# Optimization experiments

Measured on AMD Instinct MI355X. Metric: run time of the kernel, lower is better.

The kernel has to match this reference:

```python
import jax, jax.numpy as jnp
import numpy as np

B, N, M, D = 1, 16384, 16384, 3
CHUNK = 2048          # x tile size for the online-min KNN pass
NN_WEIGHT = 1.0       # self.nn_weight
# both_ways=False, free_weight=0, ch_normals_K=0 -> only cham_x branch is active


def setup_inputs() -> dict:
    key = jax.random.key(0)
    k1, k2, k3 = jax.random.split(key, 3)
    # LiDAR-like point clouds, scaled to a ~20 m scene extent
    pc1 = jax.random.normal(k1, (B, N, D), dtype=jnp.float32) * 10.0
    est_flow = jax.random.normal(k2, (B, N, D), dtype=jnp.float32) * 0.1
    pc2 = jax.random.normal(k3, (B, M, D), dtype=jnp.float32) * 10.0
    return {"pc1": pc1, "est_flow": est_flow, "pc2": pc2}


def _knn1_l1_dists(x, y):
    """Per-point min L1 distance from x [N,3] to y [M,3], tiled over x.

    Equivalent to knn_points(x, y, K=1, norm=1).dists[..., 0] without
    materializing the full [N, M] distance matrix.
    """
    n = x.shape[0]
    x_tiles = x.reshape(n // CHUNK, CHUNK, D)

    def tile_min(xc):  # xc: [CHUNK, 3]
        d = jnp.sum(jnp.abs(xc[:, None, :] - y[None, :, :]), axis=-1)  # [CHUNK, M]
        return jnp.min(d, axis=-1)                                     # [CHUNK]

    return jax.lax.map(tile_min, x_tiles).reshape(n)


def reference(pc1, est_flow, pc2):
    x = pc1 + est_flow                                   # deformed cloud [B,N,3]
    cham_x = jax.vmap(_knn1_l1_dists)(x, pc2)            # [B, N]
    cham_y = jnp.float32(0.0)                            # both_ways=False
    freespace_loss = jnp.zeros_like(cham_x)              # free_weight == 0 branch
    chamf_loss = NN_WEIGHT * (cham_x.mean() + cham_y)    # free_weight * 0 omitted
    return (chamf_loss, freespace_loss)
```

## Files before the change

### kernel.cpp

```cpp
#include <hip/hip_runtime.h>


#define TPB 256
#define RB 8
#define PTS_PER_BLOCK (TPB * RB)
#define YSEG 64
#define NITER (YSEG / 16)

typedef float sf16 __attribute__((ext_vector_type(16)));
typedef float sf8  __attribute__((ext_vector_type(8)));

#define SLOAD24(B16, B8, PTR, O16, O8)                                     \
  asm volatile("s_load_dwordx16 %0, %2, " O16 "\n\t"                       \
               "s_load_dwordx8  %1, %2, " O8                               \
               : "=s"(B16), "=s"(B8) : "s"(PTR));

#define SWAIT(B16, B8)                                                     \
  asm volatile("s_waitcnt lgkmcnt(0)" : "+s"(B16), "+s"(B8));

#define DIST2S(MR, AXv, AYv, AZv, Y0X, Y0Y, Y0Z, Y1X, Y1Y, Y1Z)           \
  {                                                                        \
    float t0, t1, t2, t3, t4;                                              \
    asm("v_sub_f32 %1, %9, %6\n\t"                                         \
        "v_sub_f32 %2, %10, %7\n\t"                                        \
        "v_sub_f32 %3, %11, %8\n\t"                                        \
        "v_sub_f32 %4, %12, %6\n\t"                                        \
        "v_sub_f32 %5, %13, %7\n\t"                                        \
        "v_add_f32 %1, |%1|, |%2|\n\t"                                     \
        "v_sub_f32 %2, %14, %8\n\t"                                        \
        "v_add_f32 %4, |%4|, |%5|\n\t"                                     \
        "v_add_f32 %1, %1, |%3|\n\t"                                       \
        "v_add_f32 %4, %4, |%2|\n\t"                                       \
        "v_min3_f32 %0, %0, %1, %4"                                        \
        : "+v"(MR), "=&v"(t0), "=&v"(t1), "=&v"(t2), "=&v"(t3), "=&v"(t4)  \
        : "v"(AXv), "v"(AYv), "v"(AZv),                                    \
          "s"(Y0X), "s"(Y0Y), "s"(Y0Z), "s"(Y1X), "s"(Y1Y), "s"(Y1Z));    \
  }

#define COMPUTE8(G16, G8)                                                  \
  {                                                                        \
    _Pragma("unroll")                                                      \
    for (int r = 0; r < RB; ++r)                                           \
      DIST2S(m[r], ax[r], ay[r], az[r],                                    \
             G16[0], G16[1], G16[2], G16[3], G16[4], G16[5]);              \
    _Pragma("unroll")                                                      \
    for (int r = 0; r < RB; ++r)                                           \
      DIST2S(m[r], ax[r], ay[r], az[r],                                    \
             G16[6], G16[7], G16[8], G16[9], G16[10], G16[11]);            \
    _Pragma("unroll")                                                      \
    for (int r = 0; r < RB; ++r)                                           \
      DIST2S(m[r], ax[r], ay[r], az[r],                                    \
             G16[12], G16[13], G16[14], G16[15], G8[0], G8[1]);            \
    _Pragma("unroll")                                                      \
    for (int r = 0; r < RB; ++r)                                           \
      DIST2S(m[r], ax[r], ay[r], az[r],                                    \
             G8[2], G8[3], G8[4], G8[5], G8[6], G8[7]);                    \
  }

__global__ __launch_bounds__(TPB) void init_kernel(unsigned* __restrict__ minbits, int N4) {
    const int i = blockIdx.x * TPB + threadIdx.x;
    uint4* p = (uint4*)minbits;
    if (i < N4) p[i] = make_uint4(0x7F7F7F7Fu, 0x7F7F7F7Fu, 0x7F7F7F7Fu, 0x7F7F7F7Fu);
}

__global__ __launch_bounds__(TPB, 8) void chamfer_kernel(
    const float* __restrict__ pc1, const float* __restrict__ flow,
    const float* __restrict__ pc2, unsigned* __restrict__ minbits,
    int N, int M) {
    const int t = threadIdx.x;

    const int ibase = blockIdx.x * PTS_PER_BLOCK + t;
    float ax[RB], ay[RB], az[RB];
#pragma unroll
    for (int r = 0; r < RB; ++r) {
        const int i = ibase + r * TPB;
        const int ic = (i < N) ? i : (N - 1);
        ax[r] = pc1[3 * ic]     + flow[3 * ic];
        ay[r] = pc1[3 * ic + 1] + flow[3 * ic + 1];
        az[r] = pc1[3 * ic + 2] + flow[3 * ic + 2];
    }

    float m[RB];
#pragma unroll
    for (int r = 0; r < RB; ++r) m[r] = 3.0e38f;

    const int ybase = blockIdx.y * YSEG;
    const int yend  = (ybase + YSEG < M) ? (ybase + YSEG) : M;

    if (yend - ybase == YSEG) {
        const float* yp = pc2 + (size_t)3 * (size_t)ybase;
        sf16 A16, B16; sf8 A8, B8;
        SLOAD24(A16, A8, yp, "0", "64");
#pragma unroll 1
        for (int it = 0; it < NITER; ++it) {
            SWAIT(A16, A8);
            SLOAD24(B16, B8, yp, "96", "160");
            COMPUTE8(A16, A8);
            SWAIT(B16, B8);
            if (it + 1 < NITER)
                SLOAD24(A16, A8, yp, "192", "256");
            COMPUTE8(B16, B8);
            yp += 48;
        }
    } else {
        for (int j = ybase; j < yend; ++j) {
            const float yx = pc2[3 * j], yy = pc2[3 * j + 1], yz = pc2[3 * j + 2];
#pragma unroll
            for (int r = 0; r < RB; ++r)
                m[r] = fminf(m[r], fabsf(ax[r] - yx) + fabsf(ay[r] - yy) + fabsf(az[r] - yz));
        }
    }

#pragma unroll
    for (int r = 0; r < RB; ++r) {
        const int i = ibase + r * TPB;
        if (i < N) atomicMin(&minbits[i], __float_as_uint(m[r]));
    }
}

__global__ __launch_bounds__(1024) void reduce_kernel(
    const unsigned* __restrict__ minbits, float* __restrict__ out,
    int N, int out_size) {
    float4* o4 = (float4*)out;
    const int n4 = out_size / 4;
    for (int k = threadIdx.x; k < n4; k += 1024)
        o4[k] = make_float4(0.f, 0.f, 0.f, 0.f);
    for (int k = n4 * 4 + threadIdx.x; k < out_size; k += 1024)
        out[k] = 0.f;

    float s = 0.0f;
    const uint4* p = (const uint4*)minbits;
    for (int k = threadIdx.x; k < N / 4; k += 1024) {
        uint4 v = p[k];
        s += __uint_as_float(v.x) + __uint_as_float(v.y) +
             __uint_as_float(v.z) + __uint_as_float(v.w);
    }
    for (int k = (N / 4) * 4 + threadIdx.x; k < N; k += 1024)
        s += __uint_as_float(minbits[k]);
#pragma unroll
    for (int off = 32; off > 0; off >>= 1) s += __shfl_down(s, off, 64);
    __shared__ float ls[16];
    const int wid = threadIdx.x >> 6, lane = threadIdx.x & 63;
    if (lane == 0) ls[wid] = s;
    __syncthreads();
    if (threadIdx.x == 0) {
        float tot = 0.0f;
        for (int w = 0; w < 16; ++w) tot += ls[w];
        out[0] = tot / (float)N;
    }
}

extern "C" void kernel_launch(void* const* d_in, const int* in_sizes, int n_in,
                              void* d_out, int out_size, void* d_ws, size_t ws_size,
                              hipStream_t stream) {
    const float* pc1  = (const float*)d_in[0];
    const float* flow = (const float*)d_in[1];
    const float* pc2  = (const float*)d_in[2];
    float* out = (float*)d_out;

    const int N = in_sizes[0] / 3;
    const int M = in_sizes[2] / 3;

    unsigned* minbits = (unsigned*)d_ws;

    const int nbN    = (N + PTS_PER_BLOCK - 1) / PTS_PER_BLOCK;
    const int msplit = (M + YSEG - 1) / YSEG;

    init_kernel<<<(N / 4 + TPB - 1) / TPB, TPB, 0, stream>>>(minbits, N / 4);
    chamfer_kernel<<<dim3(nbN, msplit), TPB, 0, stream>>>(pc1, flow, pc2, minbits, N, M);
    reduce_kernel<<<1, 1024, 0, stream>>>(minbits, out, N, out_size);
}
```

Before: 48.18 us.

## Replace atomicMin accumulation with per-segment partial mins and parallel reduction

Drops the init kernel and global atomicMin: each y-segment block writes its per-point minima to a partial buffer, and a multi-block reduce kernel takes the min across segments and produces block sums, followed by a tiny final kernel. Point rows per thread drop from 8 to 4 and the y-segment length doubles from 64 to 128. The aim is to remove atomic contention and the serial single-block reduction. In exchange it writes and rereads a 128x16384 float partial buffer (about 8 MB) and needs that much workspace.

```diff
diff --git a/kernel.cpp b/kernel.cpp
--- a/kernel.cpp
+++ b/kernel.cpp
@@ -2,9 +2,9 @@
 
 
 #define TPB 256
-#define RB 8
+#define RB 4
 #define PTS_PER_BLOCK (TPB * RB)
-#define YSEG 64
+#define YSEG 128
 #define NITER (YSEG / 16)
 
 typedef float sf16 __attribute__((ext_vector_type(16)));
@@ -57,15 +57,9 @@
              G8[2], G8[3], G8[4], G8[5], G8[6], G8[7]);                    \
   }
 
-__global__ __launch_bounds__(TPB) void init_kernel(unsigned* __restrict__ minbits, int N4) {
-    const int i = blockIdx.x * TPB + threadIdx.x;
-    uint4* p = (uint4*)minbits;
-    if (i < N4) p[i] = make_uint4(0x7F7F7F7Fu, 0x7F7F7F7Fu, 0x7F7F7F7Fu, 0x7F7F7F7Fu);
-}
-
 __global__ __launch_bounds__(TPB, 8) void chamfer_kernel(
     const float* __restrict__ pc1, const float* __restrict__ flow,
-    const float* __restrict__ pc2, unsigned* __restrict__ minbits,
+    const float* __restrict__ pc2, float* __restrict__ partial,
     int N, int M) {
     const int t = threadIdx.x;
 
@@ -111,43 +105,59 @@
         }
     }
 
+    float* __restrict__ prow = partial + (size_t)blockIdx.y * (size_t)N;
 #pragma unroll
     for (int r = 0; r < RB; ++r) {
         const int i = ibase + r * TPB;
-        if (i < N) atomicMin(&minbits[i], __float_as_uint(m[r]));
+        if (i < N) prow[i] = m[r];
     }
 }
 
-__global__ __launch_bounds__(1024) void reduce_kernel(
-    const unsigned* __restrict__ minbits, float* __restrict__ out,
-    int N, int out_size) {
-    float4* o4 = (float4*)out;
-    const int n4 = out_size / 4;
-    for (int k = threadIdx.x; k < n4; k += 1024)
-        o4[k] = make_float4(0.f, 0.f, 0.f, 0.f);
-    for (int k = n4 * 4 + threadIdx.x; k < out_size; k += 1024)
-        out[k] = 0.f;
+__global__ __launch_bounds__(256) void reduce_kernel(
+    const float* __restrict__ partial, float* __restrict__ blocksums,
+    float* __restrict__ out, int N, int S, int out_size) {
+    const int i = blockIdx.x * 256 + threadIdx.x;
+    if (1 + i < out_size) out[1 + i] = 0.0f;
 
-    float s = 0.0f;
-    const uint4* p = (const uint4*)minbits;
-    for (int k = threadIdx.x; k < N / 4; k += 1024) {
-        uint4 v = p[k];
-        s += __uint_as_float(v.x) + __uint_as_float(v.y) +
-             __uint_as_float(v.z) + __uint_as_float(v.w);
+    float v = 0.0f;
+    if (i < N) {
+        float m0 = 3.0e38f, m1 = 3.0e38f, m2 = 3.0e38f, m3 = 3.0e38f;
+        float m4 = 3.0e38f, m5 = 3.0e38f, m6 = 3.0e38f, m7 = 3.0e38f;
+        const float* p = partial + i;
+        int s = 0;
+        for (; s + 8 <= S; s += 8) {
+            m0 = fminf(m0, p[(size_t)(s + 0) * N]);
+            m1 = fminf(m1, p[(size_t)(s + 1) * N]);
+            m2 = fminf(m2, p[(size_t)(s + 2) * N]);
+            m3 = fminf(m3, p[(size_t)(s + 3) * N]);
+            m4 = fminf(m4, p[(size_t)(s + 4) * N]);
+            m5 = fminf(m5, p[(size_t)(s + 5) * N]);
+            m6 = fminf(m6, p[(size_t)(s + 6) * N]);
+            m7 = fminf(m7, p[(size_t)(s + 7) * N]);
+        }
+        for (; s < S; ++s) m0 = fminf(m0, p[(size_t)s * N]);
+        v = fminf(fminf(fminf(m0, m1), fminf(m2, m3)),
+                  fminf(fminf(m4, m5), fminf(m6, m7)));
     }
-    for (int k = (N / 4) * 4 + threadIdx.x; k < N; k += 1024)
-        s += __uint_as_float(minbits[k]);
+
+    float sv = (i < N) ? v : 0.0f;
 #pragma unroll
-    for (int off = 32; off > 0; off >>= 1) s += __shfl_down(s, off, 64);
-    __shared__ float ls[16];
+    for (int off = 32; off > 0; off >>= 1) sv += __shfl_down(sv, off, 64);
+    __shared__ float ls[4];
     const int wid = threadIdx.x >> 6, lane = threadIdx.x & 63;
-    if (lane == 0) ls[wid] = s;
+    if (lane == 0) ls[wid] = sv;
     __syncthreads();
-    if (threadIdx.x == 0) {
-        float tot = 0.0f;
-        for (int w = 0; w < 16; ++w) tot += ls[w];
-        out[0] = tot / (float)N;
-    }
+    if (threadIdx.x == 0)
+        blocksums[blockIdx.x] = ls[0] + ls[1] + ls[2] + ls[3];
+}
+
+__global__ void final_kernel(const float* __restrict__ blocksums, int nPart,
+                             float* __restrict__ out, float invN) {
+    float v = 0.0f;
+    for (int k = threadIdx.x; k < nPart; k += 64) v += blocksums[k];
+#pragma unroll
+    for (int off = 32; off > 0; off >>= 1) v += __shfl_down(v, off, 64);
+    if (threadIdx.x == 0) out[0] = v * invN;
 }
 
 extern "C" void kernel_launch(void* const* d_in, const int* in_sizes, int n_in,
@@ -161,12 +171,15 @@
     const int N = in_sizes[0] / 3;
     const int M = in_sizes[2] / 3;
 
-    unsigned* minbits = (unsigned*)d_ws;
-
     const int nbN    = (N + PTS_PER_BLOCK - 1) / PTS_PER_BLOCK;
     const int msplit = (M + YSEG - 1) / YSEG;
+    const int nb2    = (N + 255) / 256;
 
-    init_kernel<<<(N / 4 + TPB - 1) / TPB, TPB, 0, stream>>>(minbits, N / 4);
-    chamfer_kernel<<<dim3(nbN, msplit), TPB, 0, stream>>>(pc1, flow, pc2, minbits, N, M);
-    reduce_kernel<<<1, 1024, 0, stream>>>(minbits, out, N, out_size);
+    float* partial   = (float*)d_ws;
+    float* blocksums = (float*)((char*)d_ws +
+                        (size_t)msplit * (size_t)N * sizeof(float));
+
+    chamfer_kernel<<<dim3(nbN, msplit), TPB, 0, stream>>>(pc1, flow, pc2, partial, N, M);
+    reduce_kernel<<<nb2, 256, 0, stream>>>(partial, blocksums, out, N, msplit, out_size);
+    final_kernel<<<1, 64, 0, stream>>>(blocksums, nb2, out, 1.0f / (float)N);
 }
```

After: 44.76 us. 7.1% less time.

## Drop per-thread register blocking, lengthen y segments, memset init, parallel zero-fill

Applied to the files above, without the earlier changes.

Each thread now handles one x point instead of eight, and each block scans 512 y points instead of 64. The init kernel becomes a hipMemsetAsync, and the single-block reduce becomes a multi-block finalize that zeroes the output in parallel while block 0 computes the mean. This cuts atomics per point and gives more blocks in x. The cost is that each scalar y load is now reused by only one point per thread, so the kernel issues more scalar loads and loop work per distance.

```diff
diff --git a/kernel.cpp b/kernel.cpp
--- a/kernel.cpp
+++ b/kernel.cpp
@@ -2,9 +2,7 @@
 
 
 #define TPB 256
-#define RB 8
-#define PTS_PER_BLOCK (TPB * RB)
-#define YSEG 64
+#define YSEG 512
 #define NITER (YSEG / 16)
 
 typedef float sf16 __attribute__((ext_vector_type(16)));
@@ -39,29 +37,11 @@
 
 #define COMPUTE8(G16, G8)                                                  \
   {                                                                        \
-    _Pragma("unroll")                                                      \
-    for (int r = 0; r < RB; ++r)                                           \
-      DIST2S(m[r], ax[r], ay[r], az[r],                                    \
-             G16[0], G16[1], G16[2], G16[3], G16[4], G16[5]);              \
-    _Pragma("unroll")                                                      \
-    for (int r = 0; r < RB; ++r)                                           \
-      DIST2S(m[r], ax[r], ay[r], az[r],                                    \
-             G16[6], G16[7], G16[8], G16[9], G16[10], G16[11]);            \
-    _Pragma("unroll")                                                      \
-    for (int r = 0; r < RB; ++r)                                           \
-      DIST2S(m[r], ax[r], ay[r], az[r],                                    \
-             G16[12], G16[13], G16[14], G16[15], G8[0], G8[1]);            \
-    _Pragma("unroll")                                                      \
-    for (int r = 0; r < RB; ++r)                                           \
-      DIST2S(m[r], ax[r], ay[r], az[r],                                    \
-             G8[2], G8[3], G8[4], G8[5], G8[6], G8[7]);                    \
+    DIST2S(m0, ax, ay, az, G16[0], G16[1], G16[2], G16[3], G16[4], G16[5]); \
+    DIST2S(m0, ax, ay, az, G16[6], G16[7], G16[8], G16[9], G16[10], G16[11]); \
+    DIST2S(m0, ax, ay, az, G16[12], G16[13], G16[14], G16[15], G8[0], G8[1]); \
+    DIST2S(m0, ax, ay, az, G8[2], G8[3], G8[4], G8[5], G8[6], G8[7]);      \
   }
-
-__global__ __launch_bounds__(TPB) void init_kernel(unsigned* __restrict__ minbits, int N4) {
-    const int i = blockIdx.x * TPB + threadIdx.x;
-    uint4* p = (uint4*)minbits;
-    if (i < N4) p[i] = make_uint4(0x7F7F7F7Fu, 0x7F7F7F7Fu, 0x7F7F7F7Fu, 0x7F7F7F7Fu);
-}
 
 __global__ __launch_bounds__(TPB, 8) void chamfer_kernel(
     const float* __restrict__ pc1, const float* __restrict__ flow,
@@ -69,20 +49,13 @@
     int N, int M) {
     const int t = threadIdx.x;
 
-    const int ibase = blockIdx.x * PTS_PER_BLOCK + t;
-    float ax[RB], ay[RB], az[RB];
-#pragma unroll
-    for (int r = 0; r < RB; ++r) {
-        const int i = ibase + r * TPB;
-        const int ic = (i < N) ? i : (N - 1);
-        ax[r] = pc1[3 * ic]     + flow[3 * ic];
-        ay[r] = pc1[3 * ic + 1] + flow[3 * ic + 1];
-        az[r] = pc1[3 * ic + 2] + flow[3 * ic + 2];
-    }
+    const int i  = blockIdx.x * TPB + t;
+    const int ic = (i < N) ? i : (N - 1);
+    const float ax = pc1[3 * ic]     + flow[3 * ic];
+    const float ay = pc1[3 * ic + 1] + flow[3 * ic + 1];
+    const float az = pc1[3 * ic + 2] + flow[3 * ic + 2];
 
-    float m[RB];
-#pragma unroll
-    for (int r = 0; r < RB; ++r) m[r] = 3.0e38f;
+    float m0 = 3.0e38f;
 
     const int ybase = blockIdx.y * YSEG;
     const int yend  = (ybase + YSEG < M) ? (ybase + YSEG) : M;
@@ -105,48 +78,43 @@
     } else {
         for (int j = ybase; j < yend; ++j) {
             const float yx = pc2[3 * j], yy = pc2[3 * j + 1], yz = pc2[3 * j + 2];
-#pragma unroll
-            for (int r = 0; r < RB; ++r)
-                m[r] = fminf(m[r], fabsf(ax[r] - yx) + fabsf(ay[r] - yy) + fabsf(az[r] - yz));
+            m0 = fminf(m0, fabsf(ax - yx) + fabsf(ay - yy) + fabsf(az - yz));
         }
     }
 
-#pragma unroll
-    for (int r = 0; r < RB; ++r) {
-        const int i = ibase + r * TPB;
-        if (i < N) atomicMin(&minbits[i], __float_as_uint(m[r]));
-    }
+    if (i < N) atomicMin(&minbits[i], __float_as_uint(m0));
 }
 
-__global__ __launch_bounds__(1024) void reduce_kernel(
+__global__ __launch_bounds__(TPB) void finalize_kernel(
     const unsigned* __restrict__ minbits, float* __restrict__ out,
-    int N, int out_size) {
-    float4* o4 = (float4*)out;
-    const int n4 = out_size / 4;
-    for (int k = threadIdx.x; k < n4; k += 1024)
-        o4[k] = make_float4(0.f, 0.f, 0.f, 0.f);
-    for (int k = n4 * 4 + threadIdx.x; k < out_size; k += 1024)
-        out[k] = 0.f;
+    int N, int out_size, float invN) {
+    const int t = threadIdx.x;
+    const int stride = gridDim.x * TPB;
+    for (int k = blockIdx.x * TPB + t; 1 + k < out_size; k += stride)
+        out[1 + k] = 0.0f;
 
-    float s = 0.0f;
-    const uint4* p = (const uint4*)minbits;
-    for (int k = threadIdx.x; k < N / 4; k += 1024) {
-        uint4 v = p[k];
-        s += __uint_as_float(v.x) + __uint_as_float(v.y) +
-             __uint_as_float(v.z) + __uint_as_float(v.w);
-    }
-    for (int k = (N / 4) * 4 + threadIdx.x; k < N; k += 1024)
-        s += __uint_as_float(minbits[k]);
+    if (blockIdx.x == 0) {
+        float s = 0.0f;
+        const uint4* p4 = (const uint4*)minbits;
+        const int n4 = N >> 2;
+        for (int k = t; k < n4; k += TPB) {
+            uint4 v = p4[k];
+            s += __uint_as_float(v.x) + __uint_as_float(v.y) +
+                 __uint_as_float(v.z) + __uint_as_float(v.w);
+        }
+        for (int k = (n4 << 2) + t; k < N; k += TPB)
+            s += __uint_as_float(minbits[k]);
 #pragma unroll
-    for (int off = 32; off > 0; off >>= 1) s += __shfl_down(s, off, 64);
-    __shared__ float ls[16];
-    const int wid = threadIdx.x >> 6, lane = threadIdx.x & 63;
-    if (lane == 0) ls[wid] = s;
-    __syncthreads();
-    if (threadIdx.x == 0) {
-        float tot = 0.0f;
-        for (int w = 0; w < 16; ++w) tot += ls[w];
-        out[0] = tot / (float)N;
+        for (int off = 32; off > 0; off >>= 1) s += __shfl_down(s, off, 64);
+        __shared__ float ls[TPB / 64];
+        const int wid = t >> 6, lane = t & 63;
+        if (lane == 0) ls[wid] = s;
+        __syncthreads();
+        if (t == 0) {
+            float tot = 0.0f;
+            for (int w = 0; w < TPB / 64; ++w) tot += ls[w];
+            out[0] = tot * invN;
+        }
     }
 }
 
@@ -163,10 +131,12 @@
 
     unsigned* minbits = (unsigned*)d_ws;
 
-    const int nbN    = (N + PTS_PER_BLOCK - 1) / PTS_PER_BLOCK;
+    hipMemsetAsync(minbits, 0x7F, (size_t)N * sizeof(unsigned), stream);
+
+    const int nbN    = (N + TPB - 1) / TPB;
     const int msplit = (M + YSEG - 1) / YSEG;
+    const int nbF    = (out_size - 1 + TPB - 1) / TPB;
 
-    init_kernel<<<(N / 4 + TPB - 1) / TPB, TPB, 0, stream>>>(minbits, N / 4);
     chamfer_kernel<<<dim3(nbN, msplit), TPB, 0, stream>>>(pc1, flow, pc2, minbits, N, M);
-    reduce_kernel<<<1, 1024, 0, stream>>>(minbits, out, N, out_size);
+    finalize_kernel<<<nbF, TPB, 0, stream>>>(minbits, out, N, out_size, 1.0f / (float)N);
 }
```

Result: faster. 43.97 us (-8.7%).
